# Kernel tuning notes

Measured on AMD Instinct MI355X. Metric: run time of the kernel, lower is better.

The kernel has to match this reference:

```python
import jax, jax.numpy as jnp
import numpy as np

WS = 8  # window_size


def layer_norm(x, g, b, eps=1e-5):
    m = x.mean(-1, keepdims=True)
    v = x.var(-1, keepdims=True)
    return (x - m) / jnp.sqrt(v + eps) * g + b


def mamba(x, in_w, conv_w, conv_b, xproj_w, dt_w, dt_b, A_log, D_skip, out_w):
    """mamba_ssm-style Mamba block, expand=1 (d_inner == d_model), no proj biases.
    x: [B, L, D]. conv_w: [D, K] depthwise causal conv. A_log: [D, N]."""
    Bb, L, Dm = x.shape
    N = A_log.shape[1]
    K = conv_w.shape[1]
    xz = x @ in_w                                   # [B, L, 2D]
    xs, z = jnp.split(xz, 2, axis=-1)
    xp = jnp.pad(xs, ((0, 0), (K - 1, 0), (0, 0)))  # causal pad
    xc = sum(xp[:, k:k + L, :] * conv_w[:, k] for k in range(K)) + conv_b
    xc = jax.nn.silu(xc)
    dbl = xc @ xproj_w                              # [B, L, R+2N]
    R = dt_w.shape[0]
    dt, Bm, Cm = jnp.split(dbl, [R, R + N], axis=-1)
    dt = jax.nn.softplus(dt @ dt_w + dt_b)          # [B, L, D]
    A = -jnp.exp(A_log)                             # [D, N]

    def step(h, inp):
        xt, dtt, Bt, Ct = inp                       # [B,D],[B,D],[B,N],[B,N]
        h = jnp.exp(dtt[:, :, None] * A) * h + (dtt * xt)[:, :, None] * Bt[:, None, :]
        return h, jnp.einsum('bdn,bn->bd', h, Ct)

    h0 = jnp.zeros((Bb, Dm, N), x.dtype)
    _, ys = jax.lax.scan(step, h0, (xc.swapaxes(0, 1), dt.swapaxes(0, 1),
                                    Bm.swapaxes(0, 1), Cm.swapaxes(0, 1)))
    y = ys.swapaxes(0, 1) + xc * D_skip
    return (y * jax.nn.silu(z)) @ out_w


def sgfn(x, c1_w, c1_b, dw_w, dw_b, c2_w, c2_b):
    h = jnp.einsum('bchw,oc->bohw', x, c1_w) + c1_b[None, :, None, None]
    h = jax.lax.conv_general_dilated(h, dw_w, (1, 1), 'SAME',
                                     feature_group_count=dw_w.shape[0],
                                     dimension_numbers=('NCHW', 'OIHW', 'NCHW'))
    h = h + dw_b[None, :, None, None]
    h1, h2 = jnp.split(h, 2, axis=1)
    h = h1 * jax.nn.sigmoid(h2)
    return jnp.einsum('bchw,oc->bohw', h, c2_w) + c2_b[None, :, None, None]


def himamba_forward(x, r_in_w, r_conv_w, r_conv_b, r_xproj_w, r_dt_w, r_dt_b,
                    r_Alog, r_D, r_out_w, scale_mod,
                    l_in_w, l_conv_w, l_conv_b, l_xproj_w, l_dt_w, l_dt_b,
                    l_Alog, l_D, l_out_w, ln_g, ln_b,
                    c1_w, c1_b, dw_w, dw_b, c2_w, c2_b, gamma):
    B, C, H, W = x.shape
    xn_hw = layer_norm(x.transpose(0, 2, 3, 1), ln_g, ln_b)        # [B,H,W,C]
    # ---- region 4-directional scan (MHSS_SSSM_Block) ----
    x_flat = xn_hw.reshape(B, H * W, C)
    x_v = xn_hw.transpose(0, 2, 1, 3).reshape(B, H * W, C)         # column-major
    seqs = jnp.stack([x_flat, x_flat[:, ::-1], x_v, x_v[:, ::-1]])  # [4,B,L,C]
    outs = jax.vmap(mamba)(seqs, r_in_w, r_conv_w, r_conv_b, r_xproj_w,
                           r_dt_w, r_dt_b, r_Alog, r_D, r_out_w)

    def v_back(v):
        return v.reshape(B, W, H, C).transpose(0, 2, 1, 3).reshape(B, H * W, C)

    region = outs[0] + outs[1][:, ::-1] + v_back(outs[2]) + v_back(outs[3][:, ::-1])
    region = region / 4.0 * scale_mod
    x_mamba = region.reshape(B, H, W, C).transpose(0, 3, 1, 2)     # NCHW
    # ---- local windowed scan ----
    xn = xn_hw.transpose(0, 3, 1, 2)                               # NCHW
    pad_h = (-H) % WS
    pad_w = (-W) % WS
    xp = jnp.pad(xn, ((0, 0), (0, 0), (0, pad_h), (0, pad_w)))
    Hp, Wp = H + pad_h, W + pad_w
    xw = xp.reshape(B, C, Hp // WS, WS, Wp // WS, WS)
    xw = xw.transpose(0, 2, 4, 3, 5, 1).reshape(-1, WS * WS, C)
    xl = mamba(xw, l_in_w, l_conv_w, l_conv_b, l_xproj_w, l_dt_w, l_dt_b,
               l_Alog, l_D, l_out_w)
    xl = xl.reshape(B, Hp // WS, Wp // WS, WS, WS, C)
    xl = xl.transpose(0, 5, 1, 3, 2, 4).reshape(B, C, Hp, Wp)[:, :, :H, :W]
    # ---- fuse + SGFN + residual ----
    fused = x_mamba + xl
    refined = fused + sgfn(fused, c1_w, c1_b, dw_w, dw_b, c2_w, c2_b)
    return x + gamma * refined


def setup_inputs() -> dict:
    key = jax.random.key(0)
    ks = iter(jax.random.split(key, 48))
    B, C, H, W = 4, 192, 64, 64
    N_r, K_r, N_l, K_l, R = 16, 4, 8, 2, 12

    def rn(shape, s=0.02):
        return jax.random.normal(next(ks), shape, jnp.float32) * s

    return dict(
        x=jax.random.normal(next(ks), (B, C, H, W), jnp.float32),
        r_in_w=rn((4, C, 2 * C)), r_conv_w=rn((4, C, K_r), 0.2), r_conv_b=rn((4, C), 0.1),
        r_xproj_w=rn((4, C, R + 2 * N_r)), r_dt_w=rn((4, R, C), 0.1), r_dt_b=rn((4, C), 0.1),
        r_Alog=rn((4, C, N_r), 0.5), r_D=jnp.ones((4, C), jnp.float32), r_out_w=rn((4, C, C)),
        scale_mod=jnp.full((1,), 0.25, jnp.float32),
        l_in_w=rn((C, 2 * C)), l_conv_w=rn((C, K_l), 0.2), l_conv_b=rn((C,), 0.1),
        l_xproj_w=rn((C, R + 2 * N_l)), l_dt_w=rn((R, C), 0.1), l_dt_b=rn((C,), 0.1),
        l_Alog=rn((C, N_l), 0.5), l_D=jnp.ones((C,), jnp.float32), l_out_w=rn((C, C)),
        ln_g=jnp.ones((C,), jnp.float32), ln_b=jnp.zeros((C,), jnp.float32),
        c1_w=rn((4 * C, C)), c1_b=jnp.zeros((4 * C,), jnp.float32),
        dw_w=rn((4 * C, 1, 3, 3), 0.2), dw_b=jnp.zeros((4 * C,), jnp.float32),
        c2_w=rn((C, 2 * C)), c2_b=jnp.zeros((C,), jnp.float32),
        gamma=jnp.full((1,), 0.5, jnp.float32),
    )


def reference(x, r_in_w, r_conv_w, r_conv_b, r_xproj_w, r_dt_w, r_dt_b,
              r_Alog, r_D, r_out_w, scale_mod,
              l_in_w, l_conv_w, l_conv_b, l_xproj_w, l_dt_w, l_dt_b,
              l_Alog, l_D, l_out_w, ln_g, ln_b,
              c1_w, c1_b, dw_w, dw_b, c2_w, c2_b, gamma):
    return himamba_forward(x, r_in_w, r_conv_w, r_conv_b, r_xproj_w, r_dt_w, r_dt_b,
                           r_Alog, r_D, r_out_w, scale_mod,
                           l_in_w, l_conv_w, l_conv_b, l_xproj_w, l_dt_w, l_dt_b,
                           l_Alog, l_D, l_out_w, ln_g, ln_b,
                           c1_w, c1_b, dw_w, dw_b, c2_w, c2_b, gamma)
```

## Files before the change

kernel.cpp:

```cpp
#include <hip/hip_runtime.h>

typedef unsigned short ushortT;
typedef unsigned int uintT;
typedef __bf16 bf16x8 __attribute__((ext_vector_type(8)));
typedef short short8v __attribute__((ext_vector_type(8)));
typedef float f32x4 __attribute__((ext_vector_type(4)));
typedef float float4v __attribute__((ext_vector_type(4)));

#define DEV __device__ __forceinline__

DEV float sigmoidf_(float x) { return 1.f / (1.f + __expf(-x)); }
DEV float siluf_(float x)    { return x * sigmoidf_(x); }
DEV float softplusf_(float x){ return fmaxf(x, 0.f) + log1pf(__expf(-fabsf(x))); }

DEV ushortT f2bf(float f) {
  union { float f; uintT u; } x; x.f = f;
  uintT u = x.u + 0x7fffu + ((x.u >> 16) & 1u);
  return (ushortT)(u >> 16);
}
DEV float bf2f(ushortT h) {
  union { uintT u; float f; } x; x.u = ((uintT)h) << 16;
  return x.f;
}

typedef const __attribute__((address_space(1))) uintT guintT;
typedef __attribute__((address_space(3))) uintT luintT;
DEV void gl16(const void* g, void* l) {
  __builtin_amdgcn_global_load_lds((guintT*)g, (luintT*)l, 16, 0, 0);
}

__global__ __launch_bounds__(256)
void ln_kernel(const float* __restrict__ x, const float* __restrict__ g,
               const float* __restrict__ b, ushortT* __restrict__ xn) {
  const int C = 192, HW = 4096;
  __shared__ float tile[64][193];
  __shared__ float red[2][4][64];
  __shared__ float mean_s[64], rstd_s[64];
  int bb = blockIdx.x >> 6;
  int p0 = (blockIdx.x & 63) << 6;
  int tid = threadIdx.x;
  int p = tid & 63, c4 = tid >> 6;
  for (int c = c4; c < C; c += 4)
    tile[p][c] = x[((size_t)(bb * C + c)) * HW + p0 + p];
  __syncthreads();
  float s = 0.f, s2 = 0.f;
  for (int c = c4 * 48; c < c4 * 48 + 48; ++c) { float v = tile[p][c]; s += v; s2 += v * v; }
  red[0][c4][p] = s; red[1][c4][p] = s2;
  __syncthreads();
  if (c4 == 0) {
    float ss = red[0][0][p] + red[0][1][p] + red[0][2][p] + red[0][3][p];
    float qq = red[1][0][p] + red[1][1][p] + red[1][2][p] + red[1][3][p];
// ... 72 lines not shown
      for (int r = 0; r < 12; ++r)
        v += l_xproj_w[k * 28 + r] * l_dt_w[r * 192 + np];
    }
  }
  wxpc[i] = f2bf(v);
}

__global__ __launch_bounds__(256)
void prep_cw(const float* __restrict__ dw_w, const float* __restrict__ r_conv_w,
             const float* __restrict__ l_conv_w, float* __restrict__ cwt) {
  int i = blockIdx.x * 256 + threadIdx.x;
  if (i < 6912) {
    int ch = i / 9, tap = i % 9;
    cwt[tap * 768 + ch] = dw_w[i];
  } else if (i < 6912 + 3072) {
    int j = i - 6912; int d = j / 768, ch = (j % 768) / 4, k = j & 3;
    cwt[6912 + (d * 4 + k) * 192 + ch] = r_conv_w[j];
  } else if (i < 6912 + 3072 + 384) {
    int j = i - 6912 - 3072; int ch = j >> 1, k = j & 1;
    cwt[9984 + k * 192 + ch] = l_conv_w[j];
  }
}

template <int PERM> DEV int permrow(int m) {
  if (PERM == 0) return m;
  int b = m >> 12, l = m & 4095;
  if (PERM == 1) return (b << 12) | (4095 - l);
  if (PERM == 2) return (b << 12) | (((l & 63) << 6) | (l >> 6));
  if (PERM == 3) { int s = 4095 - l; return (b << 12) | (((s & 63) << 6) | (s >> 6)); }
  int ih = (m >> 9) & 7, iw = (m >> 6) & 7, p = (m >> 3) & 7, q = m & 7;
  return (b << 12) | ((((ih << 3) | p) << 6) | ((iw << 3) | q));
}
template <int PERM> DEV int permsel(int d, int m) {
  if (PERM != 5) return permrow<PERM>(m);
  switch (d) {
    case 0: return permrow<0>(m);
    case 1: return permrow<1>(m);
    case 2: return permrow<2>(m);
    default: return permrow<3>(m);
  }
}

template <int PERM, int ABF16, int EPI, int BM>
__global__ __launch_bounds__(256)
void gemm_mfma(const void* __restrict__ Ap, const ushortT* __restrict__ Bw,
               const float* __restrict__ bias, void* __restrict__ C1,
               void* __restrict__ C2, int M, int N, int K, int nGc, int cpb,
               int tilesPerDir, size_t aStr, size_t bStr, size_t c1Str, size_t c2Str,
               int split) {
  __shared__ __align__(16) ushortT As[BM * 192];
  __shared__ __align__(16) ushortT Bs[64 * 192];
  int nwg = gridDim.x;
  int bid = blockIdx.x;
  int q = nwg >> 3, r = nwg & 7, xq = bid & 7, o = bid >> 3;
  int wg = (xq < r ? xq * (q + 1) : r * (q + 1) + (xq - r) * q) + o;
  int d = wg / tilesPerDir;
  wg -= d * tilesPerDir;
  int rt = wg / nGc, cg = wg % nGc;
  int bm = rt * BM;
  const ushortT* Bwd = Bw + (size_t)d * bStr;
  int tid = threadIdx.x;
  int lane = tid & 63, w = tid >> 6;
  constexpr int MF = BM / 32;
  int wm = (w >> 1) * (MF * 16), wn = (w & 1) * 32;

  for (int cj = 0; cj < cpb; ++cj) {
    int bn = (cg * cpb + cj) * 64;
    if (bn >= N) break;
    f32x4 acc[MF][2] = {};
    for (int k0 = 0; k0 < K; k0 += 192) {
      __syncthreads();
      if (cj == 0 || K > 192) {
        if (ABF16) {
          for (int p = tid; p < BM * 24; p += 256) {
            int row = p / 24, sw = p - row * 24;
            int s = (sw & ~7) | ((sw ^ row) & 7);
            int srow = permsel<PERM>(d, bm + row);
            gl16((const ushortT*)Ap + (size_t)d * aStr + (size_t)srow * K + k0 + s * 8,
                 &As[p * 8]);
          }
        } else {
          for (int ci = tid; ci < BM * 24; ci += 256) {
            int row = ci / 24, s = ci - row * 24;
            int srow = permsel<PERM>(d, bm + row);
            int sw = (s & ~7) | ((s ^ row) & 7);
            short8v v;
            const float* af = (const float*)Ap + (size_t)d * aStr + (size_t)srow * K + k0 + s * 8;
            float4v f0 = *(const float4v*)af;
            float4v f1 = *(const float4v*)(af + 4);
#pragma unroll
            for (int j = 0; j < 4; ++j) v[j] = (short)f2bf(f0[j]);
#pragma unroll
            for (int j = 0; j < 4; ++j) v[4 + j] = (short)f2bf(f1[j]);
            *(short8v*)&As[row * 192 + sw * 8] = v;
          }
        }
      }
      for (int p = tid; p < 64 * 24; p += 256) {
        int row = p / 24, sw = p - row * 24;
        int s = (sw & ~7) | ((sw ^ row) & 7);
        int n = bn + row;
        gl16(Bwd + (size_t)n * K + k0 + s * 8, &Bs[p * 8]);
      }
      __syncthreads();
#pragma unroll
      for (int kk = 0; kk < 6; ++kk) {
        int sbase = kk * 4 + (lane >> 4);
        bf16x8 a[MF], bfr[2];
#pragma unroll
        for (int mf = 0; mf < MF; ++mf) {
          int rw = wm + mf * 16 + (lane & 15);
          int sw = (sbase & ~7) | ((sbase ^ rw) & 7);
          a[mf] = __builtin_bit_cast(bf16x8, *(const short8v*)&As[rw * 192 + sw * 8]);
        }
#pragma unroll
        for (int nf = 0; nf < 2; ++nf) {
          int rw = wn + nf * 16 + (lane & 15);
          int sw = (sbase & ~7) | ((sbase ^ rw) & 7);
          bfr[nf] = __builtin_bit_cast(bf16x8, *(const short8v*)&Bs[rw * 192 + sw * 8]);
        }
#pragma unroll
        for (int mf = 0; mf < MF; ++mf)
#pragma unroll
          for (int nf = 0; nf < 2; ++nf)
            acc[mf][nf] = __builtin_amdgcn_mfma_f32_16x16x32_bf16(a[mf], bfr[nf], acc[mf][nf], 0, 0, 0);
      }
    }
#pragma unroll
    for (int mf = 0; mf < MF; ++mf)
#pragma unroll
      for (int nf = 0; nf < 2; ++nf)
#pragma unroll
        for (int j = 0; j < 4; ++j) {
          int rowg = bm + wm + mf * 16 + ((lane >> 4) << 2) + j;
          int colg = bn + wn + nf * 16 + (lane & 15);
          if (colg >= N) continue;
          float vraw = acc[mf][nf][j];
          if (EPI == 0) {
            ((float*)C1)[(size_t)d * c1Str + (size_t)rowg * N + colg] = vraw + (bias ? bias[colg] : 0.f);
          } else if (EPI == 1) {
            ((ushortT*)C1)[(size_t)d * c1Str + (size_t)rowg * N + colg] = f2bf(vraw + (bias ? bias[colg] : 0.f));
          } else if (EPI == 2) {
            if (colg < 192) ((ushortT*)C1)[(size_t)d * c1Str + (size_t)rowg * 192 + colg] = f2bf(vraw);
            else            ((ushortT*)C2)[(size_t)d * c2Str + (size_t)rowg * 192 + colg - 192] = f2bf(vraw);
          } else {
            if (colg < split)
              ((float*)C1)[(size_t)d * c1Str + (size_t)rowg * split + colg] = vraw;
            else
              ((ushortT*)C2)[(size_t)d * c2Str + (size_t)rowg * 192 + colg - split] =
                  f2bf(softplusf_(vraw + bias[(size_t)d * 192 + colg - split]));
          }
        }
  }
}

__global__ void conv_region_k8(const ushortT* __restrict__ xs, const float* __restrict__ wt,
                               const float* __restrict__ cb, ushortT* __restrict__ out, int n8) {
  for (int i = blockIdx.x * blockDim.x + threadIdx.x; i < n8; i += gridDim.x * blockDim.x) {
    int cg = i % 24, row = i / 24;
    int c0 = cg * 8, l = row & 4095, d = row >> 14;
    const float* wtd = wt + d * 768;
    const float* cbd = cb + d * 192;
    float4v b0 = *(const float4v*)(cbd + c0), b1 = *(const float4v*)(cbd + c0 + 4);
    float acc[8] = {b0[0], b0[1], b0[2], b0[3], b1[0], b1[1], b1[2], b1[3]};
#pragma unroll
    for (int k = 0; k < 4; ++k) {
      int ls = l + k - 3;
      if (ls < 0) continue;
      short8v v = *(const short8v*)(xs + (size_t)(row + k - 3) * 192 + c0);
      float4v w0 = *(const float4v*)(wtd + k * 192 + c0);
      float4v w1 = *(const float4v*)(wtd + k * 192 + c0 + 4);
#pragma unroll
      for (int j = 0; j < 4; ++j) acc[j]     = fmaf(bf2f((ushortT)v[j]),     w0[j], acc[j]);
#pragma unroll
      for (int j = 0; j < 4; ++j) acc[4 + j] = fmaf(bf2f((ushortT)v[4 + j]), w1[j], acc[4 + j]);
    }
    short8v o;
#pragma unroll
    for (int j = 0; j < 8; ++j) o[j] = (short)f2bf(siluf_(acc[j]));
    *(short8v*)(out + (size_t)row * 192 + c0) = o;
  }
}

__global__ void conv_local_k8(const ushortT* __restrict__ xs, const float* __restrict__ wt,
                              const float* __restrict__ cb, ushortT* __restrict__ out, int n8) {
  for (int i = blockIdx.x * blockDim.x + threadIdx.x; i < n8; i += gridDim.x * blockDim.x) {
    int cg = i % 24, row = i / 24;
    int c0 = cg * 8, t = row & 63;
    float4v b0 = *(const float4v*)(cb + c0), b1 = *(const float4v*)(cb + c0 + 4);
    float acc[8] = {b0[0], b0[1], b0[2], b0[3], b1[0], b1[1], b1[2], b1[3]};
    {
      short8v v = *(const short8v*)(xs + (size_t)row * 192 + c0);
      float4v w0 = *(const float4v*)(wt + 192 + c0);
      float4v w1 = *(const float4v*)(wt + 192 + c0 + 4);
#pragma unroll
      for (int j = 0; j < 4; ++j) acc[j]     = fmaf(bf2f((ushortT)v[j]),     w0[j], acc[j]);
#pragma unroll
      for (int j = 0; j < 4; ++j) acc[4 + j] = fmaf(bf2f((ushortT)v[4 + j]), w1[j], acc[4 + j]);
    }
    if (t > 0) {
      short8v v = *(const short8v*)(xs + (size_t)(row - 1) * 192 + c0);
      float4v w0 = *(const float4v*)(wt + c0);
      float4v w1 = *(const float4v*)(wt + c0 + 4);
#pragma unroll
      for (int j = 0; j < 4; ++j) acc[j]     = fmaf(bf2f((ushortT)v[j]),     w0[j], acc[j]);
#pragma unroll
      for (int j = 0; j < 4; ++j) acc[4 + j] = fmaf(bf2f((ushortT)v[4 + j]), w1[j], acc[4 + j]);
    }
    short8v o;
#pragma unroll
    for (int j = 0; j < 8; ++j) o[j] = (short)f2bf(siluf_(acc[j]));
    *(short8v*)(out + (size_t)row * 192 + c0) = o;
  }
}

__global__ __launch_bounds__(192)
void scanA_r(const ushortT* __restrict__ xc, const float* __restrict__ dd32,
             const ushortT* __restrict__ dtv, const float* __restrict__ Alog,
             ushortT* __restrict__ Pc, ushortT* __restrict__ Hc) {
  __shared__ __align__(16) float dds[32 * 32];
  int blk = blockIdx.x;
  int chunk = blk & 127, seq = blk >> 7, dir = seq >> 2;
  int tid = threadIdx.x, c = tid;
  size_t rowbase = (size_t)seq * 4096 + chunk * 32;
  { const float4v* s = (const float4v*)(dd32 + rowbase * 32);
    for (int i = tid; i < 256; i += 192) ((float4v*)dds)[i] = s[i]; }
  float A[16], P[16], H[16];
#pragma unroll
  for (int nn = 0; nn < 16; ++nn) {
    A[nn] = -__expf(Alog[(size_t)(dir * 192 + c) * 16 + nn]);
    P[nn] = 1.f; H[nn] = 0.f;
  }
  __syncthreads();
  const ushortT* xr = xc + rowbase * 192 + c;
  const ushortT* dr = dtv + rowbase * 192 + c;
  for (int t = 0; t < 32; ++t) {
    float dtvv = bf2f(dr[t * 192]);
    float xv = bf2f(xr[t * 192]);
    float dx = dtvv * xv;
    const float* dB = dds + t * 32;
#pragma unroll
    for (int nn = 0; nn < 16; ++nn) {
      float a = __expf(dtvv * A[nn]);
      P[nn] *= a;
      H[nn] = fmaf(a, H[nn], dx * dB[nn]);
    }
  }
  size_t ob = ((size_t)(seq * 128 + chunk) * 192 + c) * 16;
  short8v p0, p1, h0, h1;
#pragma unroll
  for (int j = 0; j < 8; ++j) {
    p0[j] = (short)f2bf(P[j]); p1[j] = (short)f2bf(P[8 + j]);
    h0[j] = (short)f2bf(H[j]); h1[j] = (short)f2bf(H[8 + j]);
  }
  *(short8v*)(Pc + ob) = p0; *(short8v*)(Pc + ob + 8) = p1;
  *(short8v*)(Hc + ob) = h0; *(short8v*)(Hc + ob + 8) = h1;
}

__global__ __launch_bounds__(256)
void combine_r(ushortT* __restrict__ Pc, const ushortT* __restrict__ Hc) {
  int gid = blockIdx.x * 256 + threadIdx.x;
  int nn = gid & 15;
  int c = (gid >> 4) % 192;
  int seq = gid / (192 * 16);
  float h = 0.f;
  for (int ch = 0; ch < 128; ++ch) {
    size_t idx = (((size_t)(seq * 128 + ch) * 192 + c) << 4) + nn;
    float nh = fmaf(bf2f(Pc[idx]), h, bf2f(Hc[idx]));
    Pc[idx] = f2bf(h);
    h = nh;
  }
}

__global__ __launch_bounds__(192)
void scanC_r(const ushortT* __restrict__ xc, const float* __restrict__ dd32,
             const ushortT* __restrict__ dtv, ushortT* __restrict__ zg,
             const ushortT* __restrict__ Pc, const float* __restrict__ Alog,
             const float* __restrict__ Dskip) {
  __shared__ __align__(16) float dds[32 * 32];
  int blk = blockIdx.x;
  int chunk = blk & 127, seq = blk >> 7, dir = seq >> 2;
  int tid = threadIdx.x, c = tid;
  size_t rowbase = (size_t)seq * 4096 + chunk * 32;
  { const float4v* s = (const float4v*)(dd32 + rowbase * 32);
    for (int i = tid; i < 256; i += 192) ((float4v*)dds)[i] = s[i]; }
  float A[16], h[16];
  size_t ob = ((size_t)(seq * 128 + chunk) * 192 + c) * 16;
#pragma unroll
  for (int nn = 0; nn < 16; ++nn) {
    A[nn] = -__expf(Alog[(size_t)(dir * 192 + c) * 16 + nn]);
    h[nn] = bf2f(Pc[ob + nn]);
  }
  float Dv = Dskip[dir * 192 + c];
  __syncthreads();
  const ushortT* xr = xc + rowbase * 192 + c;
  const ushortT* dr = dtv + rowbase * 192 + c;
  ushortT* zr = zg + rowbase * 192 + c;
  for (int t = 0; t < 32; ++t) {
    float dtvv = bf2f(dr[t * 192]);
    float xv = bf2f(xr[t * 192]);
    float dx = dtvv * xv;
    const float* dB = dds + t * 32;
    float y = 0.f;
#pragma unroll
    for (int nn = 0; nn < 16; ++nn) {
      float a = __expf(dtvv * A[nn]);
      h[nn] = fmaf(a, h[nn], dx * dB[nn]);
      y = fmaf(h[nn], dB[16 + nn], y);
    }
    y = fmaf(xv, Dv, y);
    float zv = bf2f(zr[t * 192]);
    zr[t * 192] = f2bf(y * siluf_(zv));
  }
}

__global__ __launch_bounds__(192)
void scanA_l(const ushortT* __restrict__ xc, const float* __restrict__ dd16,
             const ushortT* __restrict__ dtv, const float* __restrict__ Alog,
             float* __restrict__ Pc, float* __restrict__ Hc) {
  __shared__ __align__(16) float dds[16 * 16];
  int blk = blockIdx.x;
  int chunk = blk & 3, win = blk >> 2;
  int tid = threadIdx.x, c = tid;
  size_t rowbase = (size_t)win * 64 + chunk * 16;
  { const float4v* s = (const float4v*)(dd16 + rowbase * 16);
    for (int i = tid; i < 64; i += 192) ((float4v*)dds)[i] = s[i]; }
  float A[8], P[8], H[8];
#pragma unroll
  for (int nn = 0; nn < 8; ++nn) {
    A[nn] = -__expf(Alog[(size_t)c * 8 + nn]);
    P[nn] = 1.f; H[nn] = 0.f;
  }
  __syncthreads();
  const ushortT* xr = xc + rowbase * 192 + c;
  const ushortT* dr = dtv + rowbase * 192 + c;
  for (int t = 0; t < 16; ++t) {
    float dtvv = bf2f(dr[t * 192]);
    float xv = bf2f(xr[t * 192]);
    float dx = dtvv * xv;
    const float* dB = dds + t * 16;
#pragma unroll
    for (int nn = 0; nn < 8; ++nn) {
      float a = __expf(dtvv * A[nn]);
      P[nn] *= a;
      H[nn] = fmaf(a, H[nn], dx * dB[nn]);
    }
  }
  size_t ob = ((size_t)(win * 4 + chunk) * 192 + c) * 8;
#pragma unroll
  for (int nn = 0; nn < 8; ++nn) { Pc[ob + nn] = P[nn]; Hc[ob + nn] = H[nn]; }
}

__global__ __launch_bounds__(256)
void combine_l(float* __restrict__ Pc, const float* __restrict__ Hc) {
  int gid = blockIdx.x * 256 + threadIdx.x;
  int nn = gid & 7;
  int c = (gid >> 3) % 192;
  int win = gid / (192 * 8);
  float h = 0.f;
#pragma unroll
  for (int ch = 0; ch < 4; ++ch) {
    size_t idx = (((size_t)(win * 4 + ch) * 192 + c) << 3) + nn;
    float nh = fmaf(Pc[idx], h, Hc[idx]);
    Pc[idx] = h;
    h = nh;
  }
}

__global__ __launch_bounds__(192)
void scanC_l(const ushortT* __restrict__ xc, const float* __restrict__ dd16,
             const ushortT* __restrict__ dtv, ushortT* __restrict__ zg,
             const float* __restrict__ Pc, const float* __restrict__ Alog,
             const float* __restrict__ Dskip) {
  __shared__ __align__(16) float dds[16 * 16];
  int blk = blockIdx.x;
  int chunk = blk & 3, win = blk >> 2;
  int tid = threadIdx.x, c = tid;
  size_t rowbase = (size_t)win * 64 + chunk * 16;
  { const float4v* s = (const float4v*)(dd16 + rowbase * 16);
    for (int i = tid; i < 64; i += 192) ((float4v*)dds)[i] = s[i]; }
  float A[8], h[8];
  size_t ob = ((size_t)(win * 4 + chunk) * 192 + c) * 8;
#pragma unroll
  for (int nn = 0; nn < 8; ++nn) {
    A[nn] = -__expf(Alog[(size_t)c * 8 + nn]);
    h[nn] = Pc[ob + nn];
  }
  float Dv = Dskip[c];
  __syncthreads();
  const ushortT* xr = xc + rowbase * 192 + c;
  const ushortT* dr = dtv + rowbase * 192 + c;
  ushortT* zr = zg + rowbase * 192 + c;
  for (int t = 0; t < 16; ++t) {
    float dtvv = bf2f(dr[t * 192]);
    float xv = bf2f(xr[t * 192]);
    float dx = dtvv * xv;
    const float* dB = dds + t * 16;
    float y = 0.f;
#pragma unroll
    for (int nn = 0; nn < 8; ++nn) {
      float a = __expf(dtvv * A[nn]);
      h[nn] = fmaf(a, h[nn], dx * dB[nn]);
      y = fmaf(h[nn], dB[8 + nn], y);
    }
    y = fmaf(xv, Dv, y);
    float zv = bf2f(zr[t * 192]);
    zr[t * 192] = f2bf(y * siluf_(zv));
  }
}

__global__ void combine_k8(const ushortT* __restrict__ outr, const float* __restrict__ scale_mod,
                           float* __restrict__ reg, int n8) {
  const size_t BLC = (size_t)4 * 4096 * 192;
  float sc = 0.25f * scale_mod[0];
  for (int i = blockIdx.x * blockDim.x + threadIdx.x; i < n8; i += gridDim.x * blockDim.x) {
    int cg = i % 24, row = i / 24;
    int c0 = cg * 8, l = row & 4095, b = row >> 12;
    int hh = l >> 6, ww = l & 63;
    int lv = (ww << 6) | hh;
    size_t rb = (size_t)b * 4096;
    short8v v0 = *(const short8v*)(outr + ((rb + l) * 192) + c0);
    short8v v1 = *(const short8v*)(outr + BLC + ((rb + (4095 - l)) * 192) + c0);
    short8v v2 = *(const short8v*)(outr + 2 * BLC + ((rb + lv) * 192) + c0);
    short8v v3 = *(const short8v*)(outr + 3 * BLC + ((rb + (4095 - lv)) * 192) + c0);
    float4v o0, o1;
#pragma unroll
    for (int j = 0; j < 4; ++j)
      o0[j] = (bf2f((ushortT)v0[j]) + bf2f((ushortT)v1[j]) + bf2f((ushortT)v2[j]) + bf2f((ushortT)v3[j])) * sc;
#pragma unroll
    for (int j = 0; j < 4; ++j)
      o1[j] = (bf2f((ushortT)v0[4+j]) + bf2f((ushortT)v1[4+j]) + bf2f((ushortT)v2[4+j]) + bf2f((ushortT)v3[4+j])) * sc;
    *(float4v*)(reg + (size_t)row * 192 + c0) = o0;
    *(float4v*)(reg + (size_t)row * 192 + c0 + 4) = o1;
  }
}

__global__ void fuse_k8(float* __restrict__ fused, const ushortT* __restrict__ outl, int n8) {
  for (int i = blockIdx.x * blockDim.x + threadIdx.x; i < n8; i += gridDim.x * blockDim.x) {
    int cg = i % 24, row = i / 24;
    int c0 = cg * 8, l = row & 4095, b = row >> 12;
    int hh = l >> 6, ww = l & 63;
    int win = ((b * 8 + (hh >> 3)) * 8) + (ww >> 3);
    int t = ((hh & 7) << 3) | (ww & 7);
    short8v v = *(const short8v*)(outl + ((size_t)win * 64 + t) * 192 + c0);
    float* fp = fused + (size_t)row * 192 + c0;
    float4v f0 = *(const float4v*)fp, f1 = *(const float4v*)(fp + 4);
#pragma unroll
    for (int j = 0; j < 4; ++j) f0[j] += bf2f((ushortT)v[j]);
#pragma unroll
    for (int j = 0; j < 4; ++j) f1[j] += bf2f((ushortT)v[4 + j]);
    *(float4v*)fp = f0;
    *(float4v*)(fp + 4) = f1;
  }
}

__global__ __launch_bounds__(192)
void dwglu_k(const ushortT* __restrict__ h1, const float* __restrict__ dwt,
             const float* __restrict__ dw_b, ushortT* __restrict__ glu) {
  int tid = threadIdx.x;
  int grp = tid % 48, sub = tid / 48;
  int bx = blockIdx.x;
  int b = bx >> 8, xq = (bx >> 4) & 15, ys = bx & 15;
  int x = xq * 4 + sub, y0 = ys * 4;
  int m0 = grp * 8;
  float acc1[4][8], acc2[4][8];
  {
    float4v b1a = *(const float4v*)(dw_b + m0),       b1b = *(const float4v*)(dw_b + m0 + 4);
    float4v b2a = *(const float4v*)(dw_b + 384 + m0), b2b = *(const float4v*)(dw_b + 388 + m0);
#pragma unroll
    for (int iy = 0; iy < 4; ++iy)
#pragma unroll
      for (int j = 0; j < 4; ++j) {
        acc1[iy][j] = b1a[j]; acc1[iy][4 + j] = b1b[j];
        acc2[iy][j] = b2a[j]; acc2[iy][4 + j] = b2b[j];
      }
// ... 17 lines not shown
        short8v v1 = *(const short8v*)(h1 + pix * 768 + m0);
        short8v v2 = *(const short8v*)(h1 + pix * 768 + 384 + m0);
#pragma unroll
        for (int j = 0; j < 4; ++j) {
          acc1[iy][j]     = fmaf(bf2f((ushortT)v1[j]),     w1a[j], acc1[iy][j]);
          acc1[iy][4 + j] = fmaf(bf2f((ushortT)v1[4 + j]), w1b[j], acc1[iy][4 + j]);
          acc2[iy][j]     = fmaf(bf2f((ushortT)v2[j]),     w2a[j], acc2[iy][j]);
          acc2[iy][4 + j] = fmaf(bf2f((ushortT)v2[4 + j]), w2b[j], acc2[iy][4 + j]);
        }
      }
    }
  }
#pragma unroll
  for (int iy = 0; iy < 4; ++iy) {
    size_t pix = (size_t)(b * 4096) + (y0 + iy) * 64 + x;
    short8v o;
#pragma unroll
    for (int j = 0; j < 8; ++j) o[j] = (short)f2bf(acc1[iy][j] * sigmoidf_(acc2[iy][j]));
    *(short8v*)(glu + pix * 384 + m0) = o;
  }
}

__global__ __launch_bounds__(256)
void final_k_t(const float* __restrict__ x, const float* __restrict__ fused,
               const float* __restrict__ sgout, const float* __restrict__ gamma,
               float* __restrict__ out) {
  __shared__ float tile[192][65];
  float gm = gamma[0];
  int bb = blockIdx.x >> 6;
  int p0 = (blockIdx.x & 63) << 6;
  int tid = threadIdx.x;
  for (int e = tid; e < 64 * 192; e += 256) {
    int pp = e / 192, c = e % 192;
    size_t idx = ((size_t)(bb * 4096) + p0 + pp) * 192 + c;
    tile[c][pp] = gm * (fused[idx] + sgout[idx]);
  }
  __syncthreads();
  for (int e = tid; e < 192 * 64; e += 256) {
    int c = e / 64, p = e % 64;
    size_t oi = ((size_t)(bb * 192 + c)) * 4096 + p0 + p;
    out[oi] = x[oi] + tile[c][p];
  }
}

extern "C" void kernel_launch(void* const* d_in, const int* in_sizes, int n_in,
                              void* d_out, int out_size, void* d_ws, size_t ws_size,
                              hipStream_t stream) {
  const float* x         = (const float*)d_in[0];
  const float* r_conv_w  = (const float*)d_in[2];
  const float* r_conv_b  = (const float*)d_in[3];
  const float* r_dt_w    = (const float*)d_in[5];
  const float* r_dt_b    = (const float*)d_in[6];
  const float* r_Alog    = (const float*)d_in[7];
  const float* r_D       = (const float*)d_in[8];
  const float* scale_mod = (const float*)d_in[10];
  const float* l_conv_w  = (const float*)d_in[12];
  const float* l_conv_b  = (const float*)d_in[13];
  const float* l_dt_w    = (const float*)d_in[15];
// ... 1 lines not shown
  const float* l_Alog    = (const float*)d_in[17];
  const float* l_D       = (const float*)d_in[18];
  const float* ln_g      = (const float*)d_in[20];
  const float* ln_b      = (const float*)d_in[21];
  const float* c1_b      = (const float*)d_in[23];
  const float* dw_w      = (const float*)d_in[24];
  const float* dw_b      = (const float*)d_in[25];
  const float* c2_b      = (const float*)d_in[27];
  const float* gamma     = (const float*)d_in[28];
  float* out = (float*)d_out;

  float* W = (float*)d_ws;
  const size_t BLC = (size_t)4 * 4096 * 192;
  const size_t OFF_DD  = 5 * BLC + BLC / 2;
  const size_t OFF_DTV = OFF_DD + 2097152;
  const size_t OFF_PC  = OFF_DTV + 6291456;
  const size_t OFF_HC  = OFF_PC + 3145728;
  const size_t OFF_WBF = OFF_HC + 3145728;
  const size_t OFF_WXP = OFF_WBF + 406656;
  const size_t OFF_CWT = OFF_WXP + 105984;

  ushortT* xnbf  = (ushortT*)W;
  ushortT* xcbf  = (ushortT*)(W + BLC);
  ushortT* outr  = xcbf;
  ushortT* zbf   = (ushortT*)(W + 3 * BLC);
  ushortT* xsbf  = (ushortT*)(W + 5 * BLC);
  float*   dd32  = W + OFF_DD;
  ushortT* dtvbf = (ushortT*)(W + OFF_DTV);
  ushortT* Pcb   = (ushortT*)(W + OFF_PC);
  ushortT* Hcb   = (ushortT*)(W + OFF_HC);
  ushortT* xs4   = (ushortT*)(W + OFF_PC);
  float*   Pl    = W + OFF_DTV + 1572864;
  float*   Hl    = W + OFF_DTV + 3145728;
  float*   fused = W + OFF_PC;
  ushortT* h1    = (ushortT*)W;
  ushortT* glu   = (ushortT*)(W + 4 * BLC);
  float*   sgout = W + OFF_HC;
  ushortT* wbf   = (ushortT*)(W + OFF_WBF);
  ushortT* wxpc  = (ushortT*)(W + OFF_WXP);
  float*   cwt   = W + OFF_CWT;

  auto gs = [](size_t n) { size_t g = (n + 255) / 256; return (int)(g > 8192 ? 8192 : g); };
  const int nBLC8 = (int)(BLC / 8);

  prep_w<<<(813312 + 255) / 256, 256, 0, stream>>>((const float*)d_in[1], (const float*)d_in[4],
                                                   (const float*)d_in[9], (const float*)d_in[11],
                                                   (const float*)d_in[14], (const float*)d_in[19],
                                                   (const float*)d_in[22], (const float*)d_in[26], wbf);
  prep_wxpc<<<828, 256, 0, stream>>>((const float*)d_in[4], r_dt_w,
                                     (const float*)d_in[14], l_dt_w, wxpc);
  prep_cw<<<41, 256, 0, stream>>>(dw_w, r_conv_w, l_conv_w, cwt);
  const float* dwt  = cwt;
  const float* rcwt = cwt + 6912;
  const float* lcwt = cwt + 9984;

  ln_kernel<<<dim3(256), dim3(256), 0, stream>>>(x, ln_g, ln_b, xnbf);

  const ushortT* w_in  = wbf;
  const ushortT* w_out = wbf + 328704;
  gemm_mfma<5,1,2,64><<<2048, 256, 0, stream>>>(xnbf, w_in, nullptr, xs4, zbf,
                                                16384, 384, 192, 2, 3, 512, 0, 73728, BLC, BLC, 0);
  conv_region_k8<<<6144, 256, 0, stream>>>(xs4, rcwt, r_conv_b, xcbf, 4 * nBLC8);
  gemm_mfma<0,1,3,64><<<2048, 256, 0, stream>>>(xcbf, wxpc, r_dt_b, dd32, dtvbf,
                                                16384, 224, 192, 2, 2, 512, BLC, 43008,
                                                524288, 3145728, 32);
  scanA_r<<<2048, 192, 0, stream>>>(xcbf, dd32, dtvbf, r_Alog, Pcb, Hcb);
  combine_r<<<192, 256, 0, stream>>>(Pcb, Hcb);
  scanC_r<<<2048, 192, 0, stream>>>(xcbf, dd32, dtvbf, zbf, Pcb, r_Alog, r_D);
  gemm_mfma<0,1,1,64><<<1024, 256, 0, stream>>>(zbf, w_out, nullptr, outr, nullptr,
                                                16384, 192, 192, 1, 3, 256, BLC, 36864, BLC, 0, 0);
  combine_k8<<<gs(BLC / 8), 256, 0, stream>>>(outr, scale_mod, fused, nBLC8);

  const ushortT* wl_in  = wbf + 476160;
  const ushortT* wl_out = wbf + 555264;
  const ushortT* wxpc_l = wxpc + 172032;
  gemm_mfma<4,1,2,64><<<512, 256, 0, stream>>>(xnbf, wl_in, nullptr, xsbf, zbf,
                                               16384, 384, 192, 2, 3, 512, 0, 0, 0, 0, 0);
  conv_local_k8<<<gs(BLC / 8), 256, 0, stream>>>(xsbf, lcwt, l_conv_b, xcbf, nBLC8);
  gemm_mfma<0,1,3,64><<<512, 256, 0, stream>>>(xcbf, wxpc_l, l_dt_b, dd32, dtvbf,
                                               16384, 208, 192, 2, 2, 512, 0, 0, 0, 0, 16);
  scanA_l<<<1024, 192, 0, stream>>>(xcbf, dd32, dtvbf, l_Alog, Pl, Hl);
  combine_l<<<1536, 256, 0, stream>>>(Pl, Hl);
  scanC_l<<<1024, 192, 0, stream>>>(xcbf, dd32, dtvbf, zbf, Pl, l_Alog, l_D);
  gemm_mfma<0,1,1,64><<<768, 256, 0, stream>>>(zbf, wl_out, nullptr, outr, nullptr,
                                               16384, 192, 192, 3, 1, 768, 0, 0, 0, 0, 0);
  fuse_k8<<<gs(BLC / 8), 256, 0, stream>>>(fused, outr, nBLC8);

  const ushortT* w_c1 = wbf + 592128;
  const ushortT* w_c2 = wbf + 739584;
  gemm_mfma<0,0,1,64><<<768, 256, 0, stream>>>(fused, w_c1, c1_b, h1, nullptr,
                                               16384, 768, 192, 3, 4, 768, 0, 0, 0, 0, 0);
  dwglu_k<<<1024, 192, 0, stream>>>(h1, dwt, dw_b, glu);
  gemm_mfma<0,1,0,128><<<384, 256, 0, stream>>>(glu, w_c2, c2_b, sgout, nullptr,
                                                16384, 192, 384, 3, 1, 384, 0, 0, 0, 0, 0);
  final_k_t<<<256, 256, 0, stream>>>(x, fused, sgout, gamma, out);
}
```

Measured before the change: 433.6 us.

## Keep Mamba activations in natural order and fuse combine/fuse into GEMM epilogues

Drops the per-direction row permutation from the GEMM A loads. The region in-projection becomes a single wide GEMM over natural rows, and the permutations move into the conv and scan kernels as index remapping. The four-direction output projections are now one K-concatenated GEMM whose epilogue applies the scale and writes a bf16 fused buffer. The local output GEMM accumulates into that buffer in place, which removes the separate combine and fuse elementwise kernels and the fp32 intermediate. Scan and conv accesses become strided by permutation, which can hurt coalescing for the transposed directions, and the fused residual is now stored in bf16, which lowers precision.

Measured after the change: 407.6 us. -6.0%, faster.

```diff
diff --git a/kernel.cpp b/kernel.cpp
--- a/kernel.cpp
+++ b/kernel.cpp
@@ -27,6 +27,17 @@
 typedef __attribute__((address_space(3))) uintT luintT;
 DEV void gl16(const void* g, void* l) {
   __builtin_amdgcn_global_load_lds((guintT*)g, (luintT*)l, 16, 0, 0);
+}
+
+DEV int natimg(int dir, int l) {
+  if (dir == 0) return l;
+  if (dir == 1) return 4095 - l;
+  int s = (dir == 2) ? l : (4095 - l);
+  return ((s & 63) << 6) | (s >> 6);
+}
+DEV int natwin(int m) {
+  int b = m >> 12, ih = (m >> 9) & 7, iw = (m >> 6) & 7, p = (m >> 3) & 7, q = m & 7;
+  return (b << 12) | ((((ih << 3) | p) << 6) | ((iw << 3) | q));
 }
 
 __global__ __launch_bounds__(256)
@@ -145,32 +156,14 @@
   }
 }
 
-template <int PERM> DEV int permrow(int m) {
-  if (PERM == 0) return m;
-  int b = m >> 12, l = m & 4095;
-  if (PERM == 1) return (b << 12) | (4095 - l);
-  if (PERM == 2) return (b << 12) | (((l & 63) << 6) | (l >> 6));
-  if (PERM == 3) { int s = 4095 - l; return (b << 12) | (((s & 63) << 6) | (s >> 6)); }
-  int ih = (m >> 9) & 7, iw = (m >> 6) & 7, p = (m >> 3) & 7, q = m & 7;
-  return (b << 12) | ((((ih << 3) | p) << 6) | ((iw << 3) | q));
-}
-template <int PERM> DEV int permsel(int d, int m) {
-  if (PERM != 5) return permrow<PERM>(m);
-  switch (d) {
-    case 0: return permrow<0>(m);
-    case 1: return permrow<1>(m);
-    case 2: return permrow<2>(m);
-    default: return permrow<3>(m);
-  }
-}
-
-template <int PERM, int ABF16, int EPI, int BM>
+template <int EPI, int BM, int CHUNK>
 __global__ __launch_bounds__(256)
 void gemm_mfma(const void* __restrict__ Ap, const ushortT* __restrict__ Bw,
                const float* __restrict__ bias, void* __restrict__ C1,
                void* __restrict__ C2, int M, int N, int K, int nGc, int cpb,
                int tilesPerDir, size_t aStr, size_t bStr, size_t c1Str, size_t c2Str,
                int split) {
+  const size_t BLC = (size_t)4 * 4096 * 192;
   __shared__ __align__(16) ushortT As[BM * 192];
   __shared__ __align__(16) ushortT Bs[64 * 192];
   int nwg = gridDim.x;
@@ -181,7 +174,6 @@
   wg -= d * tilesPerDir;
   int rt = wg / nGc, cg = wg % nGc;
   int bm = rt * BM;
-  const ushortT* Bwd = Bw + (size_t)d * bStr;
   int tid = threadIdx.x;
   int lane = tid & 63, w = tid >> 6;
   constexpr int MF = BM / 32;
@@ -193,37 +185,28 @@
     f32x4 acc[MF][2] = {};
     for (int k0 = 0; k0 < K; k0 += 192) {
       __syncthreads();
+      const ushortT* Abase;
+      const ushortT* Bbase;
+      int KA, KB;
+      if (CHUNK) {
+        Abase = (const ushortT*)Ap + (size_t)(k0 / 192) * aStr; KA = 192;
+        Bbase = Bw + (size_t)(k0 / 192) * bStr;                 KB = 192;
+      } else {
+        Abase = (const ushortT*)Ap + (size_t)d * aStr + k0;     KA = K;
+        Bbase = Bw + (size_t)d * bStr + k0;                     KB = K;
+      }
       if (cj == 0 || K > 192) {
-        if (ABF16) {
-          for (int p = tid; p < BM * 24; p += 256) {
-            int row = p / 24, sw = p - row * 24;
-            int s = (sw & ~7) | ((sw ^ row) & 7);
-            int srow = permsel<PERM>(d, bm + row);
-            gl16((const ushortT*)Ap + (size_t)d * aStr + (size_t)srow * K + k0 + s * 8,
-                 &As[p * 8]);
-          }
-        } else {
-          for (int ci = tid; ci < BM * 24; ci += 256) {
-            int row = ci / 24, s = ci - row * 24;
-            int srow = permsel<PERM>(d, bm + row);
-            int sw = (s & ~7) | ((s ^ row) & 7);
-            short8v v;
-            const float* af = (const float*)Ap + (size_t)d * aStr + (size_t)srow * K + k0 + s * 8;
-            float4v f0 = *(const float4v*)af;
-            float4v f1 = *(const float4v*)(af + 4);
-#pragma unroll
-            for (int j = 0; j < 4; ++j) v[j] = (short)f2bf(f0[j]);
-#pragma unroll
-            for (int j = 0; j < 4; ++j) v[4 + j] = (short)f2bf(f1[j]);
-            *(short8v*)&As[row * 192 + sw * 8] = v;
-          }
+        for (int p = tid; p < BM * 24; p += 256) {
+          int row = p / 24, sw = p - row * 24;
+          int s = (sw & ~7) | ((sw ^ row) & 7);
+          gl16(Abase + (size_t)(bm + row) * KA + s * 8, &As[p * 8]);
         }
       }
       for (int p = tid; p < 64 * 24; p += 256) {
         int row = p / 24, sw = p - row * 24;
         int s = (sw & ~7) | ((sw ^ row) & 7);
         int n = bn + row;
-        gl16(Bwd + (size_t)n * K + k0 + s * 8, &Bs[p * 8]);
+        gl16(Bbase + (size_t)n * KB + s * 8, &Bs[p * 8]);
       }
       __syncthreads();
 #pragma unroll
@@ -266,12 +249,21 @@
           } else if (EPI == 2) {
             if (colg < 192) ((ushortT*)C1)[(size_t)d * c1Str + (size_t)rowg * 192 + colg] = f2bf(vraw);
             else            ((ushortT*)C2)[(size_t)d * c2Str + (size_t)rowg * 192 + colg - 192] = f2bf(vraw);
-          } else {
+          } else if (EPI == 3) {
             if (colg < split)
               ((float*)C1)[(size_t)d * c1Str + (size_t)rowg * split + colg] = vraw;
             else
               ((ushortT*)C2)[(size_t)d * c2Str + (size_t)rowg * 192 + colg - split] =
                   f2bf(softplusf_(vraw + bias[(size_t)d * 192 + colg - split]));
+          } else if (EPI == 5) {
+            int dd2 = colg / 384, cc = colg - dd2 * 384;
+            if (cc < 192) ((ushortT*)C1)[dd2 * BLC + (size_t)rowg * 192 + cc] = f2bf(vraw);
+            else          ((ushortT*)C2)[dd2 * BLC + (size_t)rowg * 192 + cc - 192] = f2bf(vraw);
+          } else if (EPI == 6) {
+            size_t idx = (size_t)rowg * 192 + colg;
+            ((ushortT*)C1)[idx] = f2bf(bf2f(((ushortT*)C1)[idx]) + vraw);
+          } else {
+            ((ushortT*)C1)[(size_t)rowg * 192 + colg] = f2bf(vraw * (0.25f * bias[0]));
           }
         }
   }
@@ -281,16 +273,18 @@
                                const float* __restrict__ cb, ushortT* __restrict__ out, int n8) {
   for (int i = blockIdx.x * blockDim.x + threadIdx.x; i < n8; i += gridDim.x * blockDim.x) {
     int cg = i % 24, row = i / 24;
-    int c0 = cg * 8, l = row & 4095, d = row >> 14;
+    int c0 = cg * 8, d = row >> 14, l = row & 4095;
+    int base = row - l;
     const float* wtd = wt + d * 768;
     const float* cbd = cb + d * 192;
     float4v b0 = *(const float4v*)(cbd + c0), b1 = *(const float4v*)(cbd + c0 + 4);
     float acc[8] = {b0[0], b0[1], b0[2], b0[3], b1[0], b1[1], b1[2], b1[3]};
 #pragma unroll
     for (int k = 0; k < 4; ++k) {
-      int ls = l + k - 3;
-      if (ls < 0) continue;
-      short8v v = *(const short8v*)(xs + (size_t)(row + k - 3) * 192 + c0);
+      int lt = l + k - 3;
+      if (lt < 0) continue;
+      int nr = base + natimg(d, lt);
+      short8v v = *(const short8v*)(xs + (size_t)nr * 192 + c0);
       float4v w0 = *(const float4v*)(wtd + k * 192 + c0);
       float4v w1 = *(const float4v*)(wtd + k * 192 + c0 + 4);
 #pragma unroll
@@ -301,19 +295,20 @@
     short8v o;
 #pragma unroll
     for (int j = 0; j < 8; ++j) o[j] = (short)f2bf(siluf_(acc[j]));
-    *(short8v*)(out + (size_t)row * 192 + c0) = o;
+    *(short8v*)(out + (size_t)(base + natimg(d, l)) * 192 + c0) = o;
   }
 }
 
 __global__ void conv_local_k8(const ushortT* __restrict__ xs, const float* __restrict__ wt,
                               const float* __restrict__ cb, ushortT* __restrict__ out, int n8) {
   for (int i = blockIdx.x * blockDim.x + threadIdx.x; i < n8; i += gridDim.x * blockDim.x) {
-    int cg = i % 24, row = i / 24;
-    int c0 = cg * 8, t = row & 63;
+    int cg = i % 24, m = i / 24;
+    int c0 = cg * 8, t = m & 63;
+    int nr = natwin(m);
     float4v b0 = *(const float4v*)(cb + c0), b1 = *(const float4v*)(cb + c0 + 4);
     float acc[8] = {b0[0], b0[1], b0[2], b0[3], b1[0], b1[1], b1[2], b1[3]};
     {
-      short8v v = *(const short8v*)(xs + (size_t)row * 192 + c0);
+      short8v v = *(const short8v*)(xs + (size_t)nr * 192 + c0);
       float4v w0 = *(const float4v*)(wt + 192 + c0);
       float4v w1 = *(const float4v*)(wt + 192 + c0 + 4);
 #pragma unroll
@@ -322,7 +317,8 @@
       for (int j = 0; j < 4; ++j) acc[4 + j] = fmaf(bf2f((ushortT)v[4 + j]), w1[j], acc[4 + j]);
     }
     if (t > 0) {
-      short8v v = *(const short8v*)(xs + (size_t)(row - 1) * 192 + c0);
+      int np = natwin(m - 1);
+      short8v v = *(const short8v*)(xs + (size_t)np * 192 + c0);
       float4v w0 = *(const float4v*)(wt + c0);
       float4v w1 = *(const float4v*)(wt + c0 + 4);
 #pragma unroll
@@ -333,7 +329,7 @@
     short8v o;
 #pragma unroll
     for (int j = 0; j < 8; ++j) o[j] = (short)f2bf(siluf_(acc[j]));
-    *(short8v*)(out + (size_t)row * 192 + c0) = o;
+    *(short8v*)(out + (size_t)nr * 192 + c0) = o;
   }
 }
 
@@ -345,9 +341,12 @@
   int blk = blockIdx.x;
   int chunk = blk & 127, seq = blk >> 7, dir = seq >> 2;
   int tid = threadIdx.x, c = tid;
-  size_t rowbase = (size_t)seq * 4096 + chunk * 32;
-  { const float4v* s = (const float4v*)(dd32 + rowbase * 32);
-    for (int i = tid; i < 256; i += 192) ((float4v*)dds)[i] = s[i]; }
+  int seqbase = seq * 4096;
+  for (int i = tid; i < 256; i += 192) {
+    int t2 = i >> 3, part = i & 7;
+    int rr = seqbase + natimg(dir, chunk * 32 + t2);
+    ((float4v*)dds)[i] = ((const float4v*)(dd32 + (size_t)rr * 32))[part];
+  }
   float A[16], P[16], H[16];
 #pragma unroll
   for (int nn = 0; nn < 16; ++nn) {
@@ -355,11 +354,10 @@
     P[nn] = 1.f; H[nn] = 0.f;
   }
   __syncthreads();
-  const ushortT* xr = xc + rowbase * 192 + c;
-  const ushortT* dr = dtv + rowbase * 192 + c;
   for (int t = 0; t < 32; ++t) {
-    float dtvv = bf2f(dr[t * 192]);
-    float xv = bf2f(xr[t * 192]);
+    int nr = seqbase + natimg(dir, chunk * 32 + t);
+    float dtvv = bf2f(dtv[(size_t)nr * 192 + c]);
+    float xv = bf2f(xc[(size_t)nr * 192 + c]);
     float dx = dtvv * xv;
     const float* dB = dds + t * 32;
 #pragma unroll
@@ -404,9 +402,12 @@
   int blk = blockIdx.x;
   int chunk = blk & 127, seq = blk >> 7, dir = seq >> 2;
   int tid = threadIdx.x, c = tid;
-  size_t rowbase = (size_t)seq * 4096 + chunk * 32;
-  { const float4v* s = (const float4v*)(dd32 + rowbase * 32);
-    for (int i = tid; i < 256; i += 192) ((float4v*)dds)[i] = s[i]; }
+  int seqbase = seq * 4096;
+  for (int i = tid; i < 256; i += 192) {
+    int t2 = i >> 3, part = i & 7;
+    int rr = seqbase + natimg(dir, chunk * 32 + t2);
+    ((float4v*)dds)[i] = ((const float4v*)(dd32 + (size_t)rr * 32))[part];
+  }
   float A[16], h[16];
   size_t ob = ((size_t)(seq * 128 + chunk) * 192 + c) * 16;
 #pragma unroll
@@ -416,12 +417,10 @@
   }
   float Dv = Dskip[dir * 192 + c];
   __syncthreads();
-  const ushortT* xr = xc + rowbase * 192 + c;
-  const ushortT* dr = dtv + rowbase * 192 + c;
-  ushortT* zr = zg + rowbase * 192 + c;
   for (int t = 0; t < 32; ++t) {
-    float dtvv = bf2f(dr[t * 192]);
-    float xv = bf2f(xr[t * 192]);
+    int nr = seqbase + natimg(dir, chunk * 32 + t);
+    float dtvv = bf2f(dtv[(size_t)nr * 192 + c]);
+    float xv = bf2f(xc[(size_t)nr * 192 + c]);
     float dx = dtvv * xv;
     const float* dB = dds + t * 32;
     float y = 0.f;
@@ -432,8 +431,9 @@
       y = fmaf(h[nn], dB[16 + nn], y);
     }
     y = fmaf(xv, Dv, y);
-    float zv = bf2f(zr[t * 192]);
-    zr[t * 192] = f2bf(y * siluf_(zv));
+    size_t zi = (size_t)nr * 192 + c;
+    float zv = bf2f(zg[zi]);
+    zg[zi] = f2bf(y * siluf_(zv));
   }
 }
 
@@ -445,9 +445,12 @@
   int blk = blockIdx.x;
   int chunk = blk & 3, win = blk >> 2;
   int tid = threadIdx.x, c = tid;
-  size_t rowbase = (size_t)win * 64 + chunk * 16;
-  { const float4v* s = (const float4v*)(dd16 + rowbase * 16);
-    for (int i = tid; i < 64; i += 192) ((float4v*)dds)[i] = s[i]; }
+  int m0 = win * 64 + chunk * 16;
+  for (int i = tid; i < 64; i += 192) {
+    int t2 = i >> 2, part = i & 3;
+    int rr = natwin(m0 + t2);
+    ((float4v*)dds)[i] = ((const float4v*)(dd16 + (size_t)rr * 16))[part];
+  }
   float A[8], P[8], H[8];
 #pragma unroll
   for (int nn = 0; nn < 8; ++nn) {
@@ -455,11 +458,10 @@
     P[nn] = 1.f; H[nn] = 0.f;
   }
   __syncthreads();
-  const ushortT* xr = xc + rowbase * 192 + c;
-  const ushortT* dr = dtv + rowbase * 192 + c;
   for (int t = 0; t < 16; ++t) {
-    float dtvv = bf2f(dr[t * 192]);
-    float xv = bf2f(xr[t * 192]);
+    int nr = natwin(m0 + t);
+    float dtvv = bf2f(dtv[(size_t)nr * 192 + c]);
+    float xv = bf2f(xc[(size_t)nr * 192 + c]);
     float dx = dtvv * xv;
     const float* dB = dds + t * 16;
 #pragma unroll
@@ -499,9 +501,12 @@
   int blk = blockIdx.x;
   int chunk = blk & 3, win = blk >> 2;
   int tid = threadIdx.x, c = tid;
-  size_t rowbase = (size_t)win * 64 + chunk * 16;
-  { const float4v* s = (const float4v*)(dd16 + rowbase * 16);
-    for (int i = tid; i < 64; i += 192) ((float4v*)dds)[i] = s[i]; }
+  int m0 = win * 64 + chunk * 16;
+  for (int i = tid; i < 64; i += 192) {
+    int t2 = i >> 2, part = i & 3;
+    int rr = natwin(m0 + t2);
+    ((float4v*)dds)[i] = ((const float4v*)(dd16 + (size_t)rr * 16))[part];
+  }
   float A[8], h[8];
   size_t ob = ((size_t)(win * 4 + chunk) * 192 + c) * 8;
 #pragma unroll
@@ -511,12 +516,10 @@
   }
   float Dv = Dskip[c];
   __syncthreads();
-  const ushortT* xr = xc + rowbase * 192 + c;
-  const ushortT* dr = dtv + rowbase * 192 + c;
-  ushortT* zr = zg + rowbase * 192 + c;
   for (int t = 0; t < 16; ++t) {
-    float dtvv = bf2f(dr[t * 192]);
-    float xv = bf2f(xr[t * 192]);
+    int nr = natwin(m0 + t);
+    float dtvv = bf2f(dtv[(size_t)nr * 192 + c]);
+    float xv = bf2f(xc[(size_t)nr * 192 + c]);
     float dx = dtvv * xv;
     const float* dB = dds + t * 16;
     float y = 0.f;
@@ -527,53 +530,9 @@
       y = fmaf(h[nn], dB[8 + nn], y);
     }
     y = fmaf(xv, Dv, y);
-    float zv = bf2f(zr[t * 192]);
-    zr[t * 192] = f2bf(y * siluf_(zv));
-  }
-}
-
-__global__ void combine_k8(const ushortT* __restrict__ outr, const float* __restrict__ scale_mod,
-                           float* __restrict__ reg, int n8) {
-  const size_t BLC = (size_t)4 * 4096 * 192;
-  float sc = 0.25f * scale_mod[0];
-  for (int i = blockIdx.x * blockDim.x + threadIdx.x; i < n8; i += gridDim.x * blockDim.x) {
-    int cg = i % 24, row = i / 24;
-    int c0 = cg * 8, l = row & 4095, b = row >> 12;
-    int hh = l >> 6, ww = l & 63;
-    int lv = (ww << 6) | hh;
-    size_t rb = (size_t)b * 4096;
-    short8v v0 = *(const short8v*)(outr + ((rb + l) * 192) + c0);
-    short8v v1 = *(const short8v*)(outr + BLC + ((rb + (4095 - l)) * 192) + c0);
-    short8v v2 = *(const short8v*)(outr + 2 * BLC + ((rb + lv) * 192) + c0);
-    short8v v3 = *(const short8v*)(outr + 3 * BLC + ((rb + (4095 - lv)) * 192) + c0);
-    float4v o0, o1;
-#pragma unroll
-    for (int j = 0; j < 4; ++j)
-      o0[j] = (bf2f((ushortT)v0[j]) + bf2f((ushortT)v1[j]) + bf2f((ushortT)v2[j]) + bf2f((ushortT)v3[j])) * sc;
-#pragma unroll
-    for (int j = 0; j < 4; ++j)
-      o1[j] = (bf2f((ushortT)v0[4+j]) + bf2f((ushortT)v1[4+j]) + bf2f((ushortT)v2[4+j]) + bf2f((ushortT)v3[4+j])) * sc;
-    *(float4v*)(reg + (size_t)row * 192 + c0) = o0;
-    *(float4v*)(reg + (size_t)row * 192 + c0 + 4) = o1;
-  }
-}
-
-__global__ void fuse_k8(float* __restrict__ fused, const ushortT* __restrict__ outl, int n8) {
-  for (int i = blockIdx.x * blockDim.x + threadIdx.x; i < n8; i += gridDim.x * blockDim.x) {
-    int cg = i % 24, row = i / 24;
-    int c0 = cg * 8, l = row & 4095, b = row >> 12;
-    int hh = l >> 6, ww = l & 63;
-    int win = ((b * 8 + (hh >> 3)) * 8) + (ww >> 3);
-    int t = ((hh & 7) << 3) | (ww & 7);
-    short8v v = *(const short8v*)(outl + ((size_t)win * 64 + t) * 192 + c0);
-    float* fp = fused + (size_t)row * 192 + c0;
-    float4v f0 = *(const float4v*)fp, f1 = *(const float4v*)(fp + 4);
-#pragma unroll
-    for (int j = 0; j < 4; ++j) f0[j] += bf2f((ushortT)v[j]);
-#pragma unroll
-    for (int j = 0; j < 4; ++j) f1[j] += bf2f((ushortT)v[4 + j]);
-    *(float4v*)fp = f0;
-    *(float4v*)(fp + 4) = f1;
+    size_t zi = (size_t)nr * 192 + c;
+    float zv = bf2f(zg[zi]);
+    zg[zi] = f2bf(y * siluf_(zv));
   }
 }
 
@@ -637,7 +596,7 @@
 }
 
 __global__ __launch_bounds__(256)
-void final_k_t(const float* __restrict__ x, const float* __restrict__ fused,
+void final_k_t(const float* __restrict__ x, const ushortT* __restrict__ fused,
                const float* __restrict__ sgout, const float* __restrict__ gamma,
                float* __restrict__ out) {
   __shared__ float tile[192][65];
@@ -648,7 +607,7 @@
   for (int e = tid; e < 64 * 192; e += 256) {
     int pp = e / 192, c = e % 192;
     size_t idx = ((size_t)(bb * 4096) + p0 + pp) * 192 + c;
-    tile[c][pp] = gm * (fused[idx] + sgout[idx]);
+    tile[c][pp] = gm * (bf2f(fused[idx]) + sgout[idx]);
   }
   __syncthreads();
   for (int e = tid; e < 192 * 64; e += 256) {
@@ -696,7 +655,6 @@
 
   ushortT* xnbf  = (ushortT*)W;
   ushortT* xcbf  = (ushortT*)(W + BLC);
-  ushortT* outr  = xcbf;
   ushortT* zbf   = (ushortT*)(W + 3 * BLC);
   ushortT* xsbf  = (ushortT*)(W + 5 * BLC);
   float*   dd32  = W + OFF_DD;
@@ -706,7 +664,7 @@
   ushortT* xs4   = (ushortT*)(W + OFF_PC);
   float*   Pl    = W + OFF_DTV + 1572864;
   float*   Hl    = W + OFF_DTV + 3145728;
-  float*   fused = W + OFF_PC;
+  ushortT* fusedb = (ushortT*)(W + OFF_PC);
   ushortT* h1    = (ushortT*)W;
   ushortT* glu   = (ushortT*)(W + 4 * BLC);
   float*   sgout = W + OFF_HC;
@@ -732,40 +690,38 @@
 
   const ushortT* w_in  = wbf;
   const ushortT* w_out = wbf + 328704;
-  gemm_mfma<5,1,2,64><<<2048, 256, 0, stream>>>(xnbf, w_in, nullptr, xs4, zbf,
-                                                16384, 384, 192, 2, 3, 512, 0, 73728, BLC, BLC, 0);
+  gemm_mfma<5,64,0><<<1024, 256, 0, stream>>>(xnbf, w_in, nullptr, xs4, zbf,
+                                              16384, 1536, 192, 4, 6, 1024, 0, 0, 0, 0, 0);
   conv_region_k8<<<6144, 256, 0, stream>>>(xs4, rcwt, r_conv_b, xcbf, 4 * nBLC8);
-  gemm_mfma<0,1,3,64><<<2048, 256, 0, stream>>>(xcbf, wxpc, r_dt_b, dd32, dtvbf,
-                                                16384, 224, 192, 2, 2, 512, BLC, 43008,
-                                                524288, 3145728, 32);
+  gemm_mfma<3,64,0><<<2048, 256, 0, stream>>>(xcbf, wxpc, r_dt_b, dd32, dtvbf,
+                                              16384, 224, 192, 2, 2, 512, BLC, 43008,
+                                              524288, 3145728, 32);
   scanA_r<<<2048, 192, 0, stream>>>(xcbf, dd32, dtvbf, r_Alog, Pcb, Hcb);
   combine_r<<<192, 256, 0, stream>>>(Pcb, Hcb);
   scanC_r<<<2048, 192, 0, stream>>>(xcbf, dd32, dtvbf, zbf, Pcb, r_Alog, r_D);
-  gemm_mfma<0,1,1,64><<<1024, 256, 0, stream>>>(zbf, w_out, nullptr, outr, nullptr,
-                                                16384, 192, 192, 1, 3, 256, BLC, 36864, BLC, 0, 0);
-  combine_k8<<<gs(BLC / 8), 256, 0, stream>>>(outr, scale_mod, fused, nBLC8);
+  gemm_mfma<7,64,1><<<768, 256, 0, stream>>>(zbf, w_out, scale_mod, fusedb, nullptr,
+                                             16384, 192, 768, 3, 1, 768, BLC, 36864, 0, 0, 0);
 
   const ushortT* wl_in  = wbf + 476160;
   const ushortT* wl_out = wbf + 555264;
   const ushortT* wxpc_l = wxpc + 172032;
-  gemm_mfma<4,1,2,64><<<512, 256, 0, stream>>>(xnbf, wl_in, nullptr, xsbf, zbf,
-                                               16384, 384, 192, 2, 3, 512, 0, 0, 0, 0, 0);
+  gemm_mfma<2,64,0><<<512, 256, 0, stream>>>(xnbf, wl_in, nullptr, xsbf, zbf,
+                                             16384, 384, 192, 2, 3, 512, 0, 0, 0, 0, 0);
   conv_local_k8<<<gs(BLC / 8), 256, 0, stream>>>(xsbf, lcwt, l_conv_b, xcbf, nBLC8);
-  gemm_mfma<0,1,3,64><<<512, 256, 0, stream>>>(xcbf, wxpc_l, l_dt_b, dd32, dtvbf,
-                                               16384, 208, 192, 2, 2, 512, 0, 0, 0, 0, 16);
+  gemm_mfma<3,64,0><<<512, 256, 0, stream>>>(xcbf, wxpc_l, l_dt_b, dd32, dtvbf,
+                                             16384, 208, 192, 2, 2, 512, 0, 0, 0, 0, 16);
   scanA_l<<<1024, 192, 0, stream>>>(xcbf, dd32, dtvbf, l_Alog, Pl, Hl);
   combine_l<<<1536, 256, 0, stream>>>(Pl, Hl);
   scanC_l<<<1024, 192, 0, stream>>>(xcbf, dd32, dtvbf, zbf, Pl, l_Alog, l_D);
-  gemm_mfma<0,1,1,64><<<768, 256, 0, stream>>>(zbf, wl_out, nullptr, outr, nullptr,
-                                               16384, 192, 192, 3, 1, 768, 0, 0, 0, 0, 0);
-  fuse_k8<<<gs(BLC / 8), 256, 0, stream>>>(fused, outr, nBLC8);
+  gemm_mfma<6,64,0><<<768, 256, 0, stream>>>(zbf, wl_out, nullptr, fusedb, nullptr,
+                                             16384, 192, 192, 3, 1, 768, 0, 0, 0, 0, 0);
 
   const ushortT* w_c1 = wbf + 592128;
   const ushortT* w_c2 = wbf + 739584;
-  gemm_mfma<0,0,1,64><<<768, 256, 0, stream>>>(fused, w_c1, c1_b, h1, nullptr,
-                                               16384, 768, 192, 3, 4, 768, 0, 0, 0, 0, 0);
+  gemm_mfma<1,64,0><<<768, 256, 0, stream>>>(fusedb, w_c1, c1_b, h1, nullptr,
+                                             16384, 768, 192, 3, 4, 768, 0, 0, 0, 0, 0);
   dwglu_k<<<1024, 192, 0, stream>>>(h1, dwt, dw_b, glu);
-  gemm_mfma<0,1,0,128><<<384, 256, 0, stream>>>(glu, w_c2, c2_b, sgout, nullptr,
-                                                16384, 192, 384, 3, 1, 384, 0, 0, 0, 0, 0);
-  final_k_t<<<256, 256, 0, stream>>>(x, fused, sgout, gamma, out);
-}
+  gemm_mfma<0,64,0><<<768, 256, 0, stream>>>(glu, w_c2, c2_b, sgout, nullptr,
+                                             16384, 192, 384, 3, 1, 768, 0, 0, 0, 0, 0);
+  final_k_t<<<256, 256, 0, stream>>>(x, fusedb, sgout, gamma, out);
+}
```
